# Kernel optimization log

Hardware: AMD Instinct MI355X
Metric: run time of the kernel (lower is better)

## Reference

```python
import jax, jax.numpy as jnp
import numpy as np

B, DIM, HID = 16384, 1024, 2048
HALF = DIM // 2
# alternating checkerboard mask: even indices are 'masked' (conditioning) dims
_MASK = np.arange(DIM) % 2 == 0
MASK_IDX = np.nonzero(_MASK)[0]      # dims fed to the MLP (static)
NEG_IDX = np.nonzero(~_MASK)[0]      # dims transformed by the affine coupling (static)


def setup_inputs() -> dict:
    key = jax.random.key(0)
    ks = jax.random.split(key, 8)
    s = 0.02  # small init so exp(s) stays well-behaved
    return {
        "z": jax.random.normal(ks[0], (B, DIM), jnp.float32),
        "log_det": jnp.zeros((B,), jnp.float32),
        "W1": jax.random.normal(ks[1], (HID, HALF), jnp.float32) * s,
        "b1": jax.random.normal(ks[2], (HID,), jnp.float32) * s,
        "W2": jax.random.normal(ks[3], (HID, HID), jnp.float32) * s,
        "b2": jax.random.normal(ks[4], (HID,), jnp.float32) * s,
        "W3": jax.random.normal(ks[5], (DIM, HID), jnp.float32) * s,
        "b3": jax.random.normal(ks[6], (DIM,), jnp.float32) * s,
    }


def reference(z, log_det, W1, b1, W2, b2, W3, b3):
    # gather conditioning dims (static column indices -> jit-friendly)
    zm = z[:, MASK_IDX]                                    # [B, HALF]
    # 3-layer MLP with exact (erf) GELU, matching torch nn.GELU default
    h = jax.nn.gelu(zm @ W1.T + b1, approximate=False)     # [B, HID]
    h = jax.nn.gelu(h @ W2.T + b2, approximate=False)      # [B, HID]
    s_t = h @ W3.T + b3                                    # [B, DIM]
    s, t = s_t[:, :HALF], s_t[:, HALF:]                    # each [B, HALF]
    # affine coupling on the complementary dims, scatter back (forward, inverse=False)
    z_out = z.at[:, NEG_IDX].set(z[:, NEG_IDX] * jnp.exp(s) + t)
    log_det_out = log_det + jnp.sum(s, axis=1)
    return z_out, log_det_out
```

## Files before the change

kernel.cpp:

```cpp
#include <hip/hip_runtime.h>
#include <hip/hip_bf16.h>
#include <cstdint>

typedef __bf16 bf16x8 __attribute__((ext_vector_type(8)));
typedef float  f32x4  __attribute__((ext_vector_type(4)));

struct alignas(4) us2 { unsigned short x, y; };
struct alignas(8) us4 { unsigned short x, y, z, w; };

__device__ __forceinline__ unsigned short f2bf(float f) {
    union { float f; unsigned u; } a; a.f = f;
    unsigned r = a.u + 0x7fffu + ((a.u >> 16) & 1u);
    return (unsigned short)(r >> 16);
}

__device__ __forceinline__ void gl_lds16(const void* g, void* s) {
    __builtin_amdgcn_global_load_lds(
        (const __attribute__((address_space(1))) void*)g,
        (__attribute__((address_space(3))) void*)s, 16, 0, 0);
}

#define SCHEDB()  __builtin_amdgcn_sched_barrier(0)
#define SBAR()    do { SCHEDB(); __builtin_amdgcn_s_barrier(); SCHEDB(); } while (0)
#define WAITLG(N) do { asm volatile("s_waitcnt lgkmcnt(" #N ")" ::: "memory"); SCHEDB(); } while (0)
#define WAITVM(N) do { asm volatile("s_waitcnt vmcnt(" #N ")" ::: "memory"); SCHEDB(); } while (0)

template<int EPI, int K, int N>
__global__ __launch_bounds__(512, 2)
void gemm256(const unsigned short* __restrict__ A,
             const unsigned short* __restrict__ W,
             const float* __restrict__ bias,
             unsigned short* __restrict__ outb,
             float* __restrict__ outf,
             const float* __restrict__ zin,
             float* __restrict__ ldout)
{
    extern __shared__ char smem[];
    constexpr int NH = K / 32;
    constexpr int GX = N / 256;

    const int tid  = threadIdx.x;
    const int lane = tid & 63;
    const int wv   = tid >> 6;
    const int wr   = wv >> 2, wc = wv & 3;

    const int bid = blockIdx.y * GX + blockIdx.x;
    const int nwg = GX * (int)gridDim.y;
    const int swz = (bid & 7) * (nwg >> 3) + (bid >> 3);
    const size_t row0 = (size_t)(swz / GX) * 256;
    const size_t col0 = (size_t)(swz % GX) * 256;

    const int cse = (((tid & 3) ^ ((tid >> 3) & 3)) << 3);
    const unsigned short* ag = A + (row0 + (tid >> 2)) * (size_t)K + cse;
    const unsigned short* bg = W + (col0 + (tid >> 2)) * (size_t)K + cse;

    auto stage_a = [&](int hh) {
        char* dA = smem + (hh & 3) * 16384 + tid * 16;
        const unsigned short* a = ag + (size_t)hh * 32;
        gl_lds16(a,                   dA);
        gl_lds16(a + (size_t)128 * K, dA + 8192);
    };
    auto stage_b = [&](int hh) {
        char* dB = smem + (hh & 3) * 16384 + 65536 + tid * 16;
        const unsigned short* b = bg + (size_t)hh * 32;
        gl_lds16(b,                   dB);
        gl_lds16(b + (size_t)128 * K, dB + 8192);
    };

    const int ln15 = lane & 15;
    const int xo   = (((lane >> 4) ^ ((ln15 >> 1) & 3)) << 4);
    const int arow = wr * 128 + ln15;
    const int brow = wc * 64 + ln15;

#define LD(base, row) (*(const bf16x8*)((base) + (size_t)(row) * 64 + xo))

    f32x4 acc[8][4] = {};

    stage_a(0); stage_b(0);
    stage_a(1); stage_b(1);
    stage_a(2); stage_b(2);
    WAITVM(8);
    SBAR();

    for (int h = 0; h < NH; ++h) {
        const char* cA = smem + (h & 3) * 16384;
        const char* cB = cA + 65536;
        bf16x8 aL[4], aH[4], bF[4];

#pragma unroll
        for (int mf = 0; mf < 4; ++mf) aL[mf] = LD(cA, arow + mf * 16);
#pragma unroll
        for (int nf = 0; nf < 4; ++nf) bF[nf] = LD(cB, brow + nf * 16);
        if (h + 3 < NH) stage_a(h + 3);
        SBAR();
        WAITLG(0);
        __builtin_amdgcn_s_setprio(1);
#pragma unroll
        for (int mf = 0; mf < 4; ++mf)
#pragma unroll
            for (int nf = 0; nf < 4; ++nf)
                acc[mf][nf] = __builtin_amdgcn_mfma_f32_16x16x32_bf16(
                    aL[mf], bF[nf], acc[mf][nf], 0, 0, 0);
        __builtin_amdgcn_s_setprio(0);
        SBAR();

#pragma unroll
        for (int mf = 0; mf < 4; ++mf) aH[mf] = LD(cA, arow + 64 + mf * 16);
        if (h + 3 < NH) stage_b(h + 3);
        if (h < NH - 3)       WAITVM(8);
        else if (h == NH - 3) WAITVM(4);
        else if (h == NH - 2) WAITVM(0);
        SBAR();
        WAITLG(0);
        __builtin_amdgcn_s_setprio(1);
#pragma unroll
        for (int mf = 0; mf < 4; ++mf)
#pragma unroll
            for (int nf = 0; nf < 4; ++nf)
                acc[mf + 4][nf] = __builtin_amdgcn_mfma_f32_16x16x32_bf16(
                    aH[mf], bF[nf], acc[mf + 4][nf], 0, 0, 0);
        __builtin_amdgcn_s_setprio(0);
        SBAR();
    }
#undef LD

    const int lq = lane >> 4;
    float bv[4];
#pragma unroll
    for (int nf = 0; nf < 4; ++nf) bv[nf] = bias[col0 + wc * 64 + nf * 16 + ln15];

    if (EPI == 2) {
        const float2* zin2 = (const float2*)zin;
        float2*       out2 = (float2*)outf;
#pragma unroll
        for (int mi = 0; mi < 8; ++mi) {
#pragma unroll
            for (int r = 0; r < 4; ++r) {
                const size_t row = row0 + wr * 128 + mi * 16 + lq * 4 + r;
                float sv = 0.f;
#pragma unroll
                for (int p = 0; p < 2; ++p) {
                    float s = acc[mi][2 * p][r] + bv[2 * p];
                    float t = acc[mi][2 * p + 1][r] + bv[2 * p + 1];
                    const size_t j = (col0 >> 1) + wc * 32 + p * 16 + ln15;
                    float2 zv = zin2[row * 512 + j];
                    float2 o; o.x = zv.x; o.y = zv.y * __expf(s) + t;
                    out2[row * 512 + j] = o;
                    sv += s;
                }
                sv += __shfl_xor(sv, 1, 64);
                sv += __shfl_xor(sv, 2, 64);
                sv += __shfl_xor(sv, 4, 64);
                sv += __shfl_xor(sv, 8, 64);
                if (ln15 == 0) atomicAdd(&ldout[row], sv);
            }
        }
    } else {
#pragma unroll
        for (int mi = 0; mi < 8; ++mi) {
#pragma unroll
            for (int r = 0; r < 4; ++r) {
                const size_t row = row0 + wr * 128 + mi * 16 + lq * 4 + r;
#pragma unroll
                for (int nf = 0; nf < 4; ++nf) {
                    const size_t col = col0 + wc * 64 + nf * 16 + ln15;
                    float v = acc[mi][nf][r] + bv[nf];
                    if (EPI == 0) {
                        float g = 0.5f * v * (1.0f + erff(v * 0.70710678118654752f));
                        outb[row * N + col] = f2bf(g);
                    } else {
                        outf[row * N + col] = v;
                    }
                }
            }
        }
    }
}

__global__ void prep_all(const float* __restrict__ W1, const float* __restrict__ W2,
                         const float* __restrict__ W3, const float* __restrict__ b3,
                         const float* __restrict__ z,  const float* __restrict__ ld,
                         unsigned short* __restrict__ w1b, unsigned short* __restrict__ w2b,
                         unsigned short* __restrict__ w3i, float* __restrict__ b3i,
                         unsigned short* __restrict__ zm,  float* __restrict__ ldout)
{
    constexpr int N1 = 2048 * 512 / 4;
    constexpr int N2 = 2048 * 2048 / 4;
    constexpr int N3 = 1024 * 2048 / 4;
    constexpr int N4 = 16384 * 1024 / 4;
    constexpr int N5 = 1024;
    constexpr int N6 = 16384;
    constexpr int TOT = N1 + N2 + N3 + N4 + N5 + N6;
    const int stride = gridDim.x * blockDim.x;
    for (int i = blockIdx.x * blockDim.x + threadIdx.x; i < TOT; i += stride) {
        int j = i;
        if (j < N1) {
            float4 v = ((const float4*)W1)[j];
            ((us4*)w1b)[j] = us4{ f2bf(v.x), f2bf(v.y), f2bf(v.z), f2bf(v.w) };
            continue;
        }
        j -= N1;
        if (j < N2) {
            float4 v = ((const float4*)W2)[j];
            ((us4*)w2b)[j] = us4{ f2bf(v.x), f2bf(v.y), f2bf(v.z), f2bf(v.w) };
            continue;
        }
        j -= N2;
        if (j < N3) {
            int row = j >> 9, c4 = j & 511;
            int q = row >> 5, u = row & 31;
            int srcrow = (u < 16) ? (q * 16 + u) : (512 + q * 16 + u - 16);
            float4 v = ((const float4*)W3)[(size_t)srcrow * 512 + c4];
            ((us4*)w3i)[j] = us4{ f2bf(v.x), f2bf(v.y), f2bf(v.z), f2bf(v.w) };
            continue;
        }
        j -= N3;
        if (j < N4) {
            float4 v = ((const float4*)z)[j];
            ((us2*)zm)[j] = us2{ f2bf(v.x), f2bf(v.z) };
            continue;
        }
        j -= N4;
        if (j < N5) {
            int q = j >> 5, u = j & 31;
            b3i[j] = b3[(u < 16) ? (q * 16 + u) : (512 + q * 16 + u - 16)];
            continue;
        }
        j -= N5;
        ldout[j] = ld[j];
    }
}

extern "C" void kernel_launch(void* const* d_in, const int* in_sizes, int n_in,
                              void* d_out, int out_size, void* d_ws, size_t ws_size,
                              hipStream_t stream)
{
    const float* z  = (const float*)d_in[0];
    const float* ld = (const float*)d_in[1];
    const float* W1 = (const float*)d_in[2];
    const float* b1 = (const float*)d_in[3];
    const float* W2 = (const float*)d_in[4];
    const float* b2 = (const float*)d_in[5];
    const float* W3 = (const float*)d_in[6];
    const float* b3 = (const float*)d_in[7];

    float* out   = (float*)d_out;
    float* zout  = out;
    float* ldout = out + (size_t)16384 * 1024;

    char* w = (char*)d_ws;
    unsigned short* zm  = (unsigned short*)w; w += (size_t)16384 * 512 * 2;
    unsigned short* w1b = (unsigned short*)w; w += (size_t)2048 * 512 * 2;
    unsigned short* w2b = (unsigned short*)w; w += (size_t)2048 * 2048 * 2;
    unsigned short* w3i = (unsigned short*)w; w += (size_t)1024 * 2048 * 2;
    unsigned short* h1  = (unsigned short*)w; w += (size_t)16384 * 2048 * 2;
    unsigned short* h2  = (unsigned short*)w; w += (size_t)16384 * 2048 * 2;
    float*          b3i = (float*)w;          w += 1024 * 4;

    (void)hipFuncSetAttribute((const void*)&gemm256<0, 512,  2048>,
                              hipFuncAttributeMaxDynamicSharedMemorySize, 131072);
    (void)hipFuncSetAttribute((const void*)&gemm256<0, 2048, 2048>,
                              hipFuncAttributeMaxDynamicSharedMemorySize, 131072);
    (void)hipFuncSetAttribute((const void*)&gemm256<2, 2048, 1024>,
                              hipFuncAttributeMaxDynamicSharedMemorySize, 131072);

    prep_all<<<2048, 256, 0, stream>>>(W1, W2, W3, b3, z, ld,
                                       w1b, w2b, w3i, b3i, zm, ldout);

    gemm256<0, 512,  2048><<<dim3(8, 64), 512, 131072, stream>>>(zm, w1b, b1, h1, nullptr, nullptr, nullptr);
    gemm256<0, 2048, 2048><<<dim3(8, 64), 512, 131072, stream>>>(h1, w2b, b2, h2, nullptr, nullptr, nullptr);
    gemm256<2, 2048, 1024><<<dim3(4, 64), 512, 131072, stream>>>(h2, w3i, b3i, nullptr, zout, z, ldout);
}
```

Measured before the change: 327.4 us.

## Run GEMMs with 1024-thread blocks, one wave per 64x64 sub-tile

The 256x256 tile GEMM now runs with 16 waves of 1024 threads instead of 8 waves of 512. Each wave owns a 64x64 output sub-tile with 16 accumulators rather than 32. The K loop becomes a single phase per 32-wide K slice: one barrier, A and B staged together, and split lgkmcnt waits so the first MFMAs start before all fragments arrive. This aims to raise wave-level parallelism, cut per-wave register pressure and barriers per iteration, but each wave now does less MFMA work per LDS fragment load and the block is limited to one per CU.

```diff
diff --git a/kernel.cpp b/kernel.cpp
--- a/kernel.cpp
+++ b/kernel.cpp
@@ -26,7 +26,7 @@
 #define WAITVM(N) do { asm volatile("s_waitcnt vmcnt(" #N ")" ::: "memory"); SCHEDB(); } while (0)
 
 template<int EPI, int K, int N>
-__global__ __launch_bounds__(512, 2)
+__global__ __launch_bounds__(1024)
 void gemm256(const unsigned short* __restrict__ A,
              const unsigned short* __restrict__ W,
              const float* __restrict__ bias,
@@ -54,73 +54,63 @@
     const unsigned short* ag = A + (row0 + (tid >> 2)) * (size_t)K + cse;
     const unsigned short* bg = W + (col0 + (tid >> 2)) * (size_t)K + cse;
 
-    auto stage_a = [&](int hh) {
+    auto stage = [&](int hh) {
         char* dA = smem + (hh & 3) * 16384 + tid * 16;
-        const unsigned short* a = ag + (size_t)hh * 32;
-        gl_lds16(a,                   dA);
-        gl_lds16(a + (size_t)128 * K, dA + 8192);
-    };
-    auto stage_b = [&](int hh) {
-        char* dB = smem + (hh & 3) * 16384 + 65536 + tid * 16;
-        const unsigned short* b = bg + (size_t)hh * 32;
-        gl_lds16(b,                   dB);
-        gl_lds16(b + (size_t)128 * K, dB + 8192);
+        char* dB = dA + 65536;
+        gl_lds16(ag + (size_t)hh * 32, dA);
+        gl_lds16(bg + (size_t)hh * 32, dB);
     };
 
     const int ln15 = lane & 15;
     const int xo   = (((lane >> 4) ^ ((ln15 >> 1) & 3)) << 4);
-    const int arow = wr * 128 + ln15;
+    const int arow = wr * 64 + ln15;
     const int brow = wc * 64 + ln15;
 
 #define LD(base, row) (*(const bf16x8*)((base) + (size_t)(row) * 64 + xo))
 
-    f32x4 acc[8][4] = {};
-
-    stage_a(0); stage_b(0);
-    stage_a(1); stage_b(1);
-    stage_a(2); stage_b(2);
-    WAITVM(8);
-    SBAR();
+    f32x4 acc[4][4] = {};
+
+    stage(0); stage(1); stage(2);
 
     for (int h = 0; h < NH; ++h) {
         const char* cA = smem + (h & 3) * 16384;
         const char* cB = cA + 65536;
-        bf16x8 aL[4], aH[4], bF[4];
-
-#pragma unroll
-        for (int mf = 0; mf < 4; ++mf) aL[mf] = LD(cA, arow + mf * 16);
+
+        if (h <= NH - 3)      WAITVM(4);
+        else if (h == NH - 2) WAITVM(2);
+        else                  WAITVM(0);
+        SBAR();
+
+        bf16x8 aF[4], bF[4];
+        aF[0] = LD(cA, arow);
+        aF[1] = LD(cA, arow + 16);
 #pragma unroll
         for (int nf = 0; nf < 4; ++nf) bF[nf] = LD(cB, brow + nf * 16);
-        if (h + 3 < NH) stage_a(h + 3);
-        SBAR();
+        SCHEDB();
+        aF[2] = LD(cA, arow + 32);
+        aF[3] = LD(cA, arow + 48);
+        SCHEDB();
+        if (h + 3 < NH) stage(h + 3);
+
+        WAITLG(2);
+        __builtin_amdgcn_s_setprio(1);
+#pragma unroll
+        for (int mf = 0; mf < 2; ++mf)
+#pragma unroll
+            for (int nf = 0; nf < 4; ++nf)
+                acc[mf][nf] = __builtin_amdgcn_mfma_f32_16x16x32_bf16(
+                    aF[mf], bF[nf], acc[mf][nf], 0, 0, 0);
+        __builtin_amdgcn_s_setprio(0);
+
         WAITLG(0);
         __builtin_amdgcn_s_setprio(1);
 #pragma unroll
-        for (int mf = 0; mf < 4; ++mf)
+        for (int mf = 2; mf < 4; ++mf)
 #pragma unroll
             for (int nf = 0; nf < 4; ++nf)
                 acc[mf][nf] = __builtin_amdgcn_mfma_f32_16x16x32_bf16(
-                    aL[mf], bF[nf], acc[mf][nf], 0, 0, 0);
+                    aF[mf], bF[nf], acc[mf][nf], 0, 0, 0);
         __builtin_amdgcn_s_setprio(0);
-        SBAR();
-
-#pragma unroll
-        for (int mf = 0; mf < 4; ++mf) aH[mf] = LD(cA, arow + 64 + mf * 16);
-        if (h + 3 < NH) stage_b(h + 3);
-        if (h < NH - 3)       WAITVM(8);
-        else if (h == NH - 3) WAITVM(4);
-        else if (h == NH - 2) WAITVM(0);
-        SBAR();
-        WAITLG(0);
-        __builtin_amdgcn_s_setprio(1);
-#pragma unroll
-        for (int mf = 0; mf < 4; ++mf)
-#pragma unroll
-            for (int nf = 0; nf < 4; ++nf)
-                acc[mf + 4][nf] = __builtin_amdgcn_mfma_f32_16x16x32_bf16(
-                    aH[mf], bF[nf], acc[mf + 4][nf], 0, 0, 0);
-        __builtin_amdgcn_s_setprio(0);
-        SBAR();
     }
 #undef LD
 
@@ -133,10 +123,10 @@
         const float2* zin2 = (const float2*)zin;
         float2*       out2 = (float2*)outf;
 #pragma unroll
-        for (int mi = 0; mi < 8; ++mi) {
+        for (int mi = 0; mi < 4; ++mi) {
 #pragma unroll
             for (int r = 0; r < 4; ++r) {
-                const size_t row = row0 + wr * 128 + mi * 16 + lq * 4 + r;
+                const size_t row = row0 + wr * 64 + mi * 16 + lq * 4 + r;
                 float sv = 0.f;
 #pragma unroll
                 for (int p = 0; p < 2; ++p) {
@@ -157,10 +147,10 @@
         }
     } else {
 #pragma unroll
-        for (int mi = 0; mi < 8; ++mi) {
+        for (int mi = 0; mi < 4; ++mi) {
 #pragma unroll
             for (int r = 0; r < 4; ++r) {
-                const size_t row = row0 + wr * 128 + mi * 16 + lq * 4 + r;
+                const size_t row = row0 + wr * 64 + mi * 16 + lq * 4 + r;
 #pragma unroll
                 for (int nf = 0; nf < 4; ++nf) {
                     const size_t col = col0 + wc * 64 + nf * 16 + ln15;
@@ -267,7 +257,7 @@
     prep_all<<<2048, 256, 0, stream>>>(W1, W2, W3, b3, z, ld,
                                        w1b, w2b, w3i, b3i, zm, ldout);
 
-    gemm256<0, 512,  2048><<<dim3(8, 64), 512, 131072, stream>>>(zm, w1b, b1, h1, nullptr, nullptr, nullptr);
-    gemm256<0, 2048, 2048><<<dim3(8, 64), 512, 131072, stream>>>(h1, w2b, b2, h2, nullptr, nullptr, nullptr);
-    gemm256<2, 2048, 1024><<<dim3(4, 64), 512, 131072, stream>>>(h2, w3i, b3i, nullptr, zout, z, ldout);
-}
+    gemm256<0, 512,  2048><<<dim3(8, 64), 1024, 131072, stream>>>(zm, w1b, b1, h1, nullptr, nullptr, nullptr);
+    gemm256<0, 2048, 2048><<<dim3(8, 64), 1024, 131072, stream>>>(h1, w2b, b2, h2, nullptr, nullptr, nullptr);
+    gemm256<2, 2048, 1024><<<dim3(4, 64), 1024, 131072, stream>>>(h2, w3i, b3i, nullptr, zout, z, ldout);
+}
```

After: 291.6 us. 10.9% less time.
